# Kernel tuning notes

Measured on AMD Instinct MI355X. Metric: run time of the kernel, lower is better.

## Reference

```python
import jax, jax.numpy as jnp
import numpy as np

# Fixed average-trace buffer from the module (length 120)
AVG = jnp.asarray([0.0256,0.0823,0.1157,0.1315,0.1366,0.1369,0.1347,0.1308,0.1259,0.1205,0.1146,0.1086,0.1028,0.097,0.0913,0.0858,0.0805,0.0756,0.0708,0.0664,0.0623,0.0584,0.0549,0.0515,0.0485,0.0456,0.0429,0.0404,0.0381,0.036,0.034,0.0321,0.0304,0.0287,0.0272,0.0258,0.0245,0.0233,0.0222,0.0211,0.0201,0.0191,0.0182,0.0173,0.0165,0.0158,0.015,0.0143,0.0137,0.013,0.0125,0.0119,0.0114,0.0108,0.0104,0.0099,0.0095,0.0091,0.0087,0.0083,0.008,0.0077,0.0074,0.0071,0.0068,0.0065,0.0062,0.006,0.0058,0.0055,0.0053,0.005,0.0049,0.0047,0.0045,0.0044,0.0042,0.004,0.0039,0.0038,0.0036,0.0034,0.0033,0.0032,0.0031,0.003,0.0029,0.0028,0.0027,0.0026,0.0025,0.0024,0.0023,0.0022,0.0021,0.0021,0.002,0.0019,0.0018,0.0018,0.0017,0.0017,0.0016,0.0016,0.0015,0.0015,0.0014,0.0014,0.0013,0.0013,0.0013,0.0012,0.0012,0.0011,0.0011,0.0011,0.001,0.001,0.001,0.0009], dtype=jnp.float32)


def _lstm(x, w_ih, w_hh, b):
    """PyTorch-semantics single-layer LSTM. x: [N,T,D], w_ih: [4H,D], w_hh: [4H,H], b: [4H] (= b_ih + b_hh). Gate order i,f,g,o."""
    xp = jnp.einsum('ntd,gd->ntg', x, w_ih) + b  # precompute input projections: [N,T,4H]
    N = x.shape[0]
    H = w_hh.shape[1]
    h0 = jnp.zeros((N, H), x.dtype)

    def step(carry, xt):
        h, c = carry
        g = xt + h @ w_hh.T  # [N,4H]
        i, f, gg, o = jnp.split(g, 4, axis=-1)
        c = jax.nn.sigmoid(f) * c + jax.nn.sigmoid(i) * jnp.tanh(gg)
        h = jax.nn.sigmoid(o) * jnp.tanh(c)
        return (h, c), h

    _, hs = jax.lax.scan(step, (h0, h0), jnp.swapaxes(xp, 0, 1))  # hs: [T,N,H]
    return jnp.swapaxes(hs, 0, 1)  # [N,T,H]


def setup_inputs() -> dict:
    key = jax.random.key(0)
    ks = jax.random.split(key, 7)
    N, F, H = 32768, 12, 30
    s1 = 1.0 / float(np.sqrt(H))  # torch LSTM init: U(-1/sqrt(H), 1/sqrt(H))
    s2 = 1.0                      # second LSTM hidden=1 -> scale 1
    return {
        'features': jax.random.normal(ks[0], (N, F), jnp.float32),
        'w_ih1': jax.random.uniform(ks[1], (4 * H, F + 1), jnp.float32, -s1, s1),
        'w_hh1': jax.random.uniform(ks[2], (4 * H, H), jnp.float32, -s1, s1),
        'b1': jax.random.uniform(ks[3], (4 * H,), jnp.float32, -s1, s1),
        'w_ih2': jax.random.uniform(ks[4], (4, H), jnp.float32, -s2, s2),
        'w_hh2': jax.random.uniform(ks[5], (4, 1), jnp.float32, -s2, s2),
        'b2': jax.random.uniform(ks[6], (4,), jnp.float32, -s2, s2),
    }


def reference(features, w_ih1, w_hh1, b1, w_ih2, w_hh2, b2):
    N, F = features.shape
    T = AVG.shape[0]  # 120
    x = jnp.broadcast_to(features[:, None, :], (N, T, F))          # repeat features over time
    trace = jnp.broadcast_to(AVG[None, :, None], (N, T, 1))        # average trace channel
    x = jnp.concatenate([x, trace], axis=2)                        # [N,120,13]
    h1 = _lstm(x, w_ih1, w_hh1, b1)                                # [N,120,30]
    return _lstm(h1, w_ih2, w_hh2, b2)                             # [N,120,1]
```

## Files before the change

### kernel.cpp

```cpp
#include <hip/hip_runtime.h>

typedef __attribute__((ext_vector_type(8))) short bf16x8;
typedef __attribute__((ext_vector_type(4))) float f32x4;

#define LOG2E 1.44269504088896340736f

__device__ __constant__ float AVG_D[120] = {
    0.0256f,0.0823f,0.1157f,0.1315f,0.1366f,0.1369f,0.1347f,0.1308f,0.1259f,0.1205f,
    0.1146f,0.1086f,0.1028f,0.0970f,0.0913f,0.0858f,0.0805f,0.0756f,0.0708f,0.0664f,
    0.0623f,0.0584f,0.0549f,0.0515f,0.0485f,0.0456f,0.0429f,0.0404f,0.0381f,0.0360f,
    0.0340f,0.0321f,0.0304f,0.0287f,0.0272f,0.0258f,0.0245f,0.0233f,0.0222f,0.0211f,
    0.0201f,0.0191f,0.0182f,0.0173f,0.0165f,0.0158f,0.0150f,0.0143f,0.0137f,0.0130f,
    0.0125f,0.0119f,0.0114f,0.0108f,0.0104f,0.0099f,0.0095f,0.0091f,0.0087f,0.0083f,
    0.0080f,0.0077f,0.0074f,0.0071f,0.0068f,0.0065f,0.0062f,0.0060f,0.0058f,0.0055f,
    0.0053f,0.0050f,0.0049f,0.0047f,0.0045f,0.0044f,0.0042f,0.0040f,0.0039f,0.0038f,
    0.0036f,0.0034f,0.0033f,0.0032f,0.0031f,0.0030f,0.0029f,0.0028f,0.0027f,0.0026f,
    0.0025f,0.0024f,0.0023f,0.0022f,0.0021f,0.0021f,0.0020f,0.0019f,0.0018f,0.0018f,
    0.0017f,0.0017f,0.0016f,0.0016f,0.0015f,0.0015f,0.0014f,0.0014f,0.0013f,0.0013f,
    0.0013f,0.0012f,0.0012f,0.0011f,0.0011f,0.0011f,0.0010f,0.0010f,0.0010f,0.0009f
};

__device__ __forceinline__ float sig2(float x) {
    return __builtin_amdgcn_rcpf(1.0f + __builtin_amdgcn_exp2f(x));
}
__device__ __forceinline__ float tanh2(float x) {
    return fmaf(2.0f, __builtin_amdgcn_rcpf(1.0f + __builtin_amdgcn_exp2f(x)), -1.0f);
}
__device__ __forceinline__ unsigned short tb(float x) {
    return (unsigned short)(__float_as_uint(x) >> 16);
}
__device__ __forceinline__ float fb(unsigned short h) {
    return __uint_as_float(((unsigned)h) << 16);
}

__global__ void pack_weights(const float* __restrict__ w_ih1,
                             const float* __restrict__ w_hh1,
                             const float* __restrict__ b1,
                             const float* __restrict__ w_ih2,
                             const float* __restrict__ b2,
                             float* __restrict__ ws) {
    unsigned short* whi = (unsigned short*)ws;
    unsigned short* wlo = (unsigned short*)(ws + 2048);
    float* bconst = ws + 4096;
    float* wih1f  = ws + 4224;
    unsigned* avgpk = (unsigned*)(ws + 5760);
    const int tid = threadIdx.x;
    for (int idx = tid; idx < 4096; idx += 256) {
        const int T = idx >> 9, lane = (idx >> 3) & 63, j = idx & 7;
        const int r = 16 * T + (lane & 15);
        const int k = ((lane >> 4) & 3) * 8 + j;
        const int u = r >> 2, q = r & 3;
        const float sc = (q == 2) ? (-2.0f * LOG2E) : (-LOG2E);
        float v = 0.0f;
        if (u < 30) {
            if (k < 30)       v = w_hh1[(q * 30 + u) * 30 + k];
            else if (k == 30) v = w_ih1[(q * 30 + u) * 13 + 12];
        } else if (u == 30 && k < 30) {
            v = w_ih2[q * 30 + k];
        }
        v *= sc;
        const unsigned short hi = tb(v);
        whi[idx] = hi;
        wlo[idx] = tb(v - fb(hi));
    }
    for (int r = tid; r < 128; r += 256) {
        const int u = r >> 2, q = r & 3;
        const float sc = (q == 2) ? (-2.0f * LOG2E) : (-LOG2E);
        bconst[r] = sc * ((u < 30) ? b1[q * 30 + u] : ((u == 30) ? b2[q] : 0.0f));
    }
    for (int idx = tid; idx < 1536; idx += 256) {
        const int r = idx / 12, d = idx % 12;
        const int u = r >> 2, q = r & 3;
        const float sc = (q == 2) ? (-2.0f * LOG2E) : (-LOG2E);
        wih1f[idx] = (u < 30) ? sc * w_ih1[(q * 30 + u) * 13 + d] : 0.0f;
    }
    for (int t = tid; t < 121; t += 256) {
        const float a = (t < 120) ? AVG_D[t] : 0.0f;
        const unsigned short hi = tb(a);
        const unsigned short lo = tb(a - fb(hi));
        avgpk[t] = (unsigned)hi | ((unsigned)lo << 16);
    }
}

__global__ __launch_bounds__(128, 4)
void lstm_mfma_kernel(const float* __restrict__ feat,
                      const float* __restrict__ w_hh2,
                      const float* __restrict__ ws,
                      float* __restrict__ out) {
    __shared__ __align__(16) unsigned short hhi[2][16 * 40];
    __shared__ __align__(16) unsigned short hlo[2][16 * 40];
    __shared__ __align__(16) float out_s[16 * 124];

    const int tid  = threadIdx.x;
    const int lane = tid & 63;
    const int wv   = __builtin_amdgcn_readfirstlane(tid >> 6) & 1;
    const int s    = lane & 15;
    const int quad = lane >> 4;
    const int seq  = blockIdx.x * 16 + s;
    const unsigned* avgpk = (const unsigned*)(ws + 5760);

    {
        unsigned* zh = (unsigned*)(&hhi[0][0]);
        unsigned* zl = (unsigned*)(&hlo[0][0]);
        for (int i = tid; i < 640; i += 128) { zh[i] = 0u; zl[i] = 0u; }
    }
    __syncthreads();
    if (tid < 16) {
        const unsigned a0 = avgpk[0];
        hhi[0][tid * 40 + 30] = (unsigned short)a0;
        hlo[0][tid * 40 + 30] = (unsigned short)(a0 >> 16);
    }

    bf16x8 Ahi[4], Alo[4];
    {
        const unsigned short* wahi = (const unsigned short*)ws;
        const unsigned short* walo = (const unsigned short*)(ws + 2048);
#pragma unroll
        for (int T = 0; T < 4; T++) {
            const int Tg = 4 * wv + T;
            Ahi[T] = *(const bf16x8*)(wahi + Tg * 512 + lane * 8);
            Alo[T] = *(const bf16x8*)(walo + Tg * 512 + lane * 8);
        }
    }

    float f0[12];
    {
        const float4* fp = reinterpret_cast<const float4*>(feat + seq * 12);
        float4 A = fp[0], B = fp[1], C = fp[2];
        f0[0]=A.x; f0[1]=A.y; f0[2]=A.z; f0[3]=A.w;
        f0[4]=B.x; f0[5]=B.y; f0[6]=B.z; f0[7]=B.w;
        f0[8]=C.x; f0[9]=C.y; f0[10]=C.z; f0[11]=C.w;
    }
    f32x4 projb[4];
    {
        const float* bconst = ws + 4096;
        const float* wih1f  = ws + 4224;
#pragma unroll
        for (int T = 0; T < 4; T++) {
#pragma unroll
            for (int g = 0; g < 4; g++) {
                const int r = 16 * (4 * wv + T) + 4 * quad + g;
                float acc = bconst[r];
#pragma unroll
                for (int d = 0; d < 12; d++) acc = fmaf(f0[d], wih1f[r * 12 + d], acc);
                projb[T][g] = acc;
            }
        }
    }

    float c1[4];
#pragma unroll
    for (int T = 0; T < 4; T++) c1[T] = 0.0f;
    float h2 = 0.0f, c2 = 0.0f;
    const float whs0 = -LOG2E * w_hh2[0];
    const float whs1 = -LOG2E * w_hh2[1];
    const float whs2 = -2.0f * LOG2E * w_hh2[2];
    const float whs3 = -LOG2E * w_hh2[3];

    __syncthreads();

    unsigned apk_cur = avgpk[1];

#pragma unroll 1
    for (int t = 0; t <= 120; t++) {
        const int buf = t & 1;
        const unsigned short* bh = hhi[buf];
        const unsigned short* bl = hlo[buf];
        unsigned short* nh = hhi[buf ^ 1];
        unsigned short* nl = hlo[buf ^ 1];

        const unsigned apk = apk_cur;
        apk_cur = avgpk[(t + 2 <= 120) ? (t + 2) : 120];

        const bf16x8 Bhi = *(const bf16x8*)(bh + s * 40 + 8 * quad);
        const bf16x8 Blo = *(const bf16x8*)(bl + s * 40 + 8 * quad);

        f32x4 D[4];
#pragma unroll
        for (int T = 0; T < 4; T++)
            D[T] = __builtin_amdgcn_mfma_f32_16x16x32_bf16(Alo[T], Bhi, projb[T], 0, 0, 0);
#pragma unroll
        for (int T = 0; T < 4; T++)
            D[T] = __builtin_amdgcn_mfma_f32_16x16x32_bf16(Ahi[T], Blo, D[T], 0, 0, 0);
#pragma unroll
        for (int T = 0; T < 4; T++)
            D[T] = __builtin_amdgcn_mfma_f32_16x16x32_bf16(Ahi[T], Bhi, D[T], 0, 0, 0);

        if (wv == 1 && t >= 1 && quad == 2) {
            const float g0 = fmaf(h2, whs0, D[3][0]);
            const float g1 = fmaf(h2, whs1, D[3][1]);
            const float g2 = fmaf(h2, whs2, D[3][2]);
            const float g3 = fmaf(h2, whs3, D[3][3]);
            c2 = sig2(g1) * c2 + sig2(g0) * tanh2(g2);
            h2 = sig2(g3) * tanh2(c2 * (-2.0f * LOG2E));
            out_s[s * 124 + (t - 1)] = h2;
        }

        if (t < 120) {
            float s2a[4], Ba[4], hka[4];
#pragma unroll
            for (int T = 0; T < 4; T++) {
                const float ei = __builtin_amdgcn_exp2f(D[T][0]);
                const float ef = __builtin_amdgcn_exp2f(D[T][1]);
                const float eg = __builtin_amdgcn_exp2f(D[T][2]);
                const float eo = __builtin_amdgcn_exp2f(D[T][3]);
                const float pi_ = 1.0f + ei, pf = 1.0f + ef;
                const float pg  = 1.0f + eg, po = 1.0f + eo;
                const float pig = pi_ * pg;
                const float num = fmaf(c1[T], pig, (1.0f - eg) * pf);
                const float ck  = num * __builtin_amdgcn_rcpf(pf * pig);
                c1[T] = ck;
                float carg = -2.0f * LOG2E * ck;
                carg = fminf(fmaxf(carg, -20.0f), 20.0f);
                const float ec = __builtin_amdgcn_exp2f(carg);
                s2a[T] = 1.0f - ec;
                Ba[T]  = po * (1.0f + ec);
            }
            {
                const float P01 = __builtin_amdgcn_rcpf(Ba[0] * Ba[1]);
                hka[0] = s2a[0] * (Ba[1] * P01);
                hka[1] = s2a[1] * (Ba[0] * P01);
                const int u3 = 16 * wv + 12 + quad;
                const float B3e = (u3 < 30) ? Ba[3] : 1.0f;
                const float P23 = __builtin_amdgcn_rcpf(Ba[2] * B3e);
                hka[2] = s2a[2] * (B3e * P23);
                hka[3] = s2a[3] * (Ba[2] * P23);
            }
#pragma unroll
            for (int T = 0; T < 4; T++) {
                const int u = 16 * wv + 4 * T + quad;
                const unsigned hbits = __float_as_uint(hka[T]);
                const float rem = hka[T] - __uint_as_float(hbits & 0xffff0000u);
                unsigned hi16 = hbits >> 16;
                unsigned lo16 = __float_as_uint(rem) >> 16;
                if (T == 3) {
                    if (u == 30) { hi16 = apk & 0xffffu; lo16 = apk >> 16; }
                    else if (u == 31) { hi16 = 0u; lo16 = 0u; }
                }
                nh[s * 40 + u] = (unsigned short)hi16;
                nl[s * 40 + u] = (unsigned short)lo16;
            }
            __syncthreads();
        }
    }

    __syncthreads();
    float* outb = out + (size_t)blockIdx.x * 16 * 120;
#pragma unroll
    for (int it = 0; it < 4; it++) {
        const int fi = it * 128 + tid;
        if (fi < 480) {
            const int sq = fi / 30, j = fi % 30;
            const float4 v = *reinterpret_cast<const float4*>(&out_s[sq * 124 + j * 4]);
            *reinterpret_cast<float4*>(&outb[sq * 120 + j * 4]) = v;
        }
    }
}

extern "C" void kernel_launch(void* const* d_in, const int* in_sizes, int n_in,
                              void* d_out, int out_size, void* d_ws, size_t ws_size,
                              hipStream_t stream) {
    (void)in_sizes; (void)n_in; (void)out_size; (void)ws_size;
    const float* feat  = (const float*)d_in[0];
    const float* w_ih1 = (const float*)d_in[1];
    const float* w_hh1 = (const float*)d_in[2];
    const float* b1    = (const float*)d_in[3];
    const float* w_ih2 = (const float*)d_in[4];
    const float* w_hh2 = (const float*)d_in[5];
    const float* b2    = (const float*)d_in[6];
    float* ws  = (float*)d_ws;
    float* out = (float*)d_out;

    hipLaunchKernelGGL(pack_weights, dim3(1), dim3(256), 0, stream,
                       w_ih1, w_hh1, b1, w_ih2, b2, ws);
    hipLaunchKernelGGL(lstm_mfma_kernel, dim3(2048), dim3(128), 0, stream,
                       feat, w_hh2, ws, out);
}
```

Measured before the change: 246.1 us.

## Process two independent 16-sequence groups per block to interleave MFMA chains

Each block now handles 32 sequences as two independent groups A and B. Their MFMA chains and gate math are interleaved inside one timestep, so one barrier per step covers both groups and the serial dependency latency of each group can overlap with the other. Grid size is halved, launch bounds drop to 2 blocks per CU, and the second-layer update moves after the barrier. The cost is roughly double the register and shared-memory use per block, which may lower occupancy.

```diff
diff --git a/kernel.cpp b/kernel.cpp
--- a/kernel.cpp
+++ b/kernel.cpp
@@ -82,33 +82,39 @@
     }
 }
 
-__global__ __launch_bounds__(128, 4)
+__global__ __launch_bounds__(128, 2)
 void lstm_mfma_kernel(const float* __restrict__ feat,
                       const float* __restrict__ w_hh2,
                       const float* __restrict__ ws,
                       float* __restrict__ out) {
-    __shared__ __align__(16) unsigned short hhi[2][16 * 40];
-    __shared__ __align__(16) unsigned short hlo[2][16 * 40];
-    __shared__ __align__(16) float out_s[16 * 124];
+    __shared__ __align__(16) unsigned short hhiA[2][16 * 40];
+    __shared__ __align__(16) unsigned short hloA[2][16 * 40];
+    __shared__ __align__(16) unsigned short hhiB[2][16 * 40];
+    __shared__ __align__(16) unsigned short hloB[2][16 * 40];
+    __shared__ __align__(16) float out_s[32 * 124];
 
     const int tid  = threadIdx.x;
     const int lane = tid & 63;
     const int wv   = __builtin_amdgcn_readfirstlane(tid >> 6) & 1;
     const int s    = lane & 15;
     const int quad = lane >> 4;
-    const int seq  = blockIdx.x * 16 + s;
+    const int seqA = blockIdx.x * 32 + s;
     const unsigned* avgpk = (const unsigned*)(ws + 5760);
 
     {
-        unsigned* zh = (unsigned*)(&hhi[0][0]);
-        unsigned* zl = (unsigned*)(&hlo[0][0]);
-        for (int i = tid; i < 640; i += 128) { zh[i] = 0u; zl[i] = 0u; }
+        unsigned* z0 = (unsigned*)(&hhiA[0][0]);
+        unsigned* z1 = (unsigned*)(&hloA[0][0]);
+        unsigned* z2 = (unsigned*)(&hhiB[0][0]);
+        unsigned* z3 = (unsigned*)(&hloB[0][0]);
+        for (int i = tid; i < 640; i += 128) { z0[i]=0u; z1[i]=0u; z2[i]=0u; z3[i]=0u; }
     }
     __syncthreads();
     if (tid < 16) {
         const unsigned a0 = avgpk[0];
-        hhi[0][tid * 40 + 30] = (unsigned short)a0;
-        hlo[0][tid * 40 + 30] = (unsigned short)(a0 >> 16);
+        hhiA[0][tid * 40 + 30] = (unsigned short)a0;
+        hloA[0][tid * 40 + 30] = (unsigned short)(a0 >> 16);
+        hhiB[0][tid * 40 + 30] = (unsigned short)a0;
+        hloB[0][tid * 40 + 30] = (unsigned short)(a0 >> 16);
     }
 
     bf16x8 Ahi[4], Alo[4];
@@ -123,35 +129,45 @@
         }
     }
 
-    float f0[12];
-    {
-        const float4* fp = reinterpret_cast<const float4*>(feat + seq * 12);
-        float4 A = fp[0], B = fp[1], C = fp[2];
-        f0[0]=A.x; f0[1]=A.y; f0[2]=A.z; f0[3]=A.w;
-        f0[4]=B.x; f0[5]=B.y; f0[6]=B.z; f0[7]=B.w;
-        f0[8]=C.x; f0[9]=C.y; f0[10]=C.z; f0[11]=C.w;
-    }
-    f32x4 projb[4];
+    f32x4 projbA[4], projbB[4];
     {
         const float* bconst = ws + 4096;
         const float* wih1f  = ws + 4224;
+        float f0[12], g0[12];
+        {
+            const float4* fp = reinterpret_cast<const float4*>(feat + seqA * 12);
+            float4 A = fp[0], B = fp[1], C = fp[2];
+            f0[0]=A.x; f0[1]=A.y; f0[2]=A.z; f0[3]=A.w;
+            f0[4]=B.x; f0[5]=B.y; f0[6]=B.z; f0[7]=B.w;
+            f0[8]=C.x; f0[9]=C.y; f0[10]=C.z; f0[11]=C.w;
+            const float4* gp = reinterpret_cast<const float4*>(feat + (seqA + 16) * 12);
+            float4 D_ = gp[0], E = gp[1], F = gp[2];
+            g0[0]=D_.x; g0[1]=D_.y; g0[2]=D_.z; g0[3]=D_.w;
+            g0[4]=E.x; g0[5]=E.y; g0[6]=E.z; g0[7]=E.w;
+            g0[8]=F.x; g0[9]=F.y; g0[10]=F.z; g0[11]=F.w;
+        }
 #pragma unroll
         for (int T = 0; T < 4; T++) {
 #pragma unroll
             for (int g = 0; g < 4; g++) {
                 const int r = 16 * (4 * wv + T) + 4 * quad + g;
-                float acc = bconst[r];
-#pragma unroll
-                for (int d = 0; d < 12; d++) acc = fmaf(f0[d], wih1f[r * 12 + d], acc);
-                projb[T][g] = acc;
-            }
-        }
-    }
-
-    float c1[4];
-#pragma unroll
-    for (int T = 0; T < 4; T++) c1[T] = 0.0f;
-    float h2 = 0.0f, c2 = 0.0f;
+                float accA = bconst[r], accB = bconst[r];
+#pragma unroll
+                for (int d = 0; d < 12; d++) {
+                    const float w = wih1f[r * 12 + d];
+                    accA = fmaf(f0[d], w, accA);
+                    accB = fmaf(g0[d], w, accB);
+                }
+                projbA[T][g] = accA;
+                projbB[T][g] = accB;
+            }
+        }
+    }
+
+    float c1A[4], c1B[4];
+#pragma unroll
+    for (int T = 0; T < 4; T++) { c1A[T] = 0.0f; c1B[T] = 0.0f; }
+    float h2A = 0.0f, c2A = 0.0f, h2B = 0.0f, c2B = 0.0f;
     const float whs0 = -LOG2E * w_hh2[0];
     const float whs1 = -LOG2E * w_hh2[1];
     const float whs2 = -2.0f * LOG2E * w_hh2[2];
@@ -164,59 +180,61 @@
 #pragma unroll 1
     for (int t = 0; t <= 120; t++) {
         const int buf = t & 1;
-        const unsigned short* bh = hhi[buf];
-        const unsigned short* bl = hlo[buf];
-        unsigned short* nh = hhi[buf ^ 1];
-        unsigned short* nl = hlo[buf ^ 1];
+        const unsigned short* bhA = hhiA[buf];
+        const unsigned short* blA = hloA[buf];
+        unsigned short* nhA = hhiA[buf ^ 1];
+        unsigned short* nlA = hloA[buf ^ 1];
+        const unsigned short* bhB = hhiB[buf];
+        const unsigned short* blB = hloB[buf];
+        unsigned short* nhB = hhiB[buf ^ 1];
+        unsigned short* nlB = hloB[buf ^ 1];
 
         const unsigned apk = apk_cur;
         apk_cur = avgpk[(t + 2 <= 120) ? (t + 2) : 120];
 
-        const bf16x8 Bhi = *(const bf16x8*)(bh + s * 40 + 8 * quad);
-        const bf16x8 Blo = *(const bf16x8*)(bl + s * 40 + 8 * quad);
-
-        f32x4 D[4];
-#pragma unroll
-        for (int T = 0; T < 4; T++)
-            D[T] = __builtin_amdgcn_mfma_f32_16x16x32_bf16(Alo[T], Bhi, projb[T], 0, 0, 0);
-#pragma unroll
-        for (int T = 0; T < 4; T++)
-            D[T] = __builtin_amdgcn_mfma_f32_16x16x32_bf16(Ahi[T], Blo, D[T], 0, 0, 0);
-#pragma unroll
-        for (int T = 0; T < 4; T++)
-            D[T] = __builtin_amdgcn_mfma_f32_16x16x32_bf16(Ahi[T], Bhi, D[T], 0, 0, 0);
-
-        if (wv == 1 && t >= 1 && quad == 2) {
-            const float g0 = fmaf(h2, whs0, D[3][0]);
-            const float g1 = fmaf(h2, whs1, D[3][1]);
-            const float g2 = fmaf(h2, whs2, D[3][2]);
-            const float g3 = fmaf(h2, whs3, D[3][3]);
-            c2 = sig2(g1) * c2 + sig2(g0) * tanh2(g2);
-            h2 = sig2(g3) * tanh2(c2 * (-2.0f * LOG2E));
-            out_s[s * 124 + (t - 1)] = h2;
+        const bf16x8 BhiA = *(const bf16x8*)(bhA + s * 40 + 8 * quad);
+        const bf16x8 BloA = *(const bf16x8*)(blA + s * 40 + 8 * quad);
+        const bf16x8 BhiB = *(const bf16x8*)(bhB + s * 40 + 8 * quad);
+        const bf16x8 BloB = *(const bf16x8*)(blB + s * 40 + 8 * quad);
+
+        f32x4 DA[4], DB[4];
+#pragma unroll
+        for (int T = 0; T < 4; T++) {
+            DA[T] = __builtin_amdgcn_mfma_f32_16x16x32_bf16(Alo[T], BhiA, projbA[T], 0, 0, 0);
+            DB[T] = __builtin_amdgcn_mfma_f32_16x16x32_bf16(Alo[T], BhiB, projbB[T], 0, 0, 0);
+        }
+#pragma unroll
+        for (int T = 0; T < 4; T++) {
+            DA[T] = __builtin_amdgcn_mfma_f32_16x16x32_bf16(Ahi[T], BloA, DA[T], 0, 0, 0);
+            DB[T] = __builtin_amdgcn_mfma_f32_16x16x32_bf16(Ahi[T], BloB, DB[T], 0, 0, 0);
+        }
+#pragma unroll
+        for (int T = 0; T < 4; T++) {
+            DA[T] = __builtin_amdgcn_mfma_f32_16x16x32_bf16(Ahi[T], BhiA, DA[T], 0, 0, 0);
+            DB[T] = __builtin_amdgcn_mfma_f32_16x16x32_bf16(Ahi[T], BhiB, DB[T], 0, 0, 0);
         }
 
         if (t < 120) {
-            float s2a[4], Ba[4], hka[4];
-#pragma unroll
-            for (int T = 0; T < 4; T++) {
-                const float ei = __builtin_amdgcn_exp2f(D[T][0]);
-                const float ef = __builtin_amdgcn_exp2f(D[T][1]);
-                const float eg = __builtin_amdgcn_exp2f(D[T][2]);
-                const float eo = __builtin_amdgcn_exp2f(D[T][3]);
-                const float pi_ = 1.0f + ei, pf = 1.0f + ef;
-                const float pg  = 1.0f + eg, po = 1.0f + eo;
-                const float pig = pi_ * pg;
-                const float num = fmaf(c1[T], pig, (1.0f - eg) * pf);
-                const float ck  = num * __builtin_amdgcn_rcpf(pf * pig);
-                c1[T] = ck;
-                float carg = -2.0f * LOG2E * ck;
-                carg = fminf(fmaxf(carg, -20.0f), 20.0f);
-                const float ec = __builtin_amdgcn_exp2f(carg);
-                s2a[T] = 1.0f - ec;
-                Ba[T]  = po * (1.0f + ec);
-            }
             {
+                float s2a[4], Ba[4], hka[4];
+#pragma unroll
+                for (int T = 0; T < 4; T++) {
+                    const float ei = __builtin_amdgcn_exp2f(DA[T][0]);
+                    const float ef = __builtin_amdgcn_exp2f(DA[T][1]);
+                    const float eg = __builtin_amdgcn_exp2f(DA[T][2]);
+                    const float eo = __builtin_amdgcn_exp2f(DA[T][3]);
+                    const float pi_ = 1.0f + ei, pf = 1.0f + ef;
+                    const float pg  = 1.0f + eg, po = 1.0f + eo;
+                    const float pig = pi_ * pg;
+                    const float num = fmaf(c1A[T], pig, (1.0f - eg) * pf);
+                    const float ck  = num * __builtin_amdgcn_rcpf(pf * pig);
+                    c1A[T] = ck;
+                    float carg = -2.0f * LOG2E * ck;
+                    carg = fminf(fmaxf(carg, -20.0f), 20.0f);
+                    const float ec = __builtin_amdgcn_exp2f(carg);
+                    s2a[T] = 1.0f - ec;
+                    Ba[T]  = po * (1.0f + ec);
+                }
                 const float P01 = __builtin_amdgcn_rcpf(Ba[0] * Ba[1]);
                 hka[0] = s2a[0] * (Ba[1] * P01);
                 hka[1] = s2a[1] * (Ba[0] * P01);
@@ -225,31 +243,96 @@
                 const float P23 = __builtin_amdgcn_rcpf(Ba[2] * B3e);
                 hka[2] = s2a[2] * (B3e * P23);
                 hka[3] = s2a[3] * (Ba[2] * P23);
-            }
-#pragma unroll
-            for (int T = 0; T < 4; T++) {
-                const int u = 16 * wv + 4 * T + quad;
-                const unsigned hbits = __float_as_uint(hka[T]);
-                const float rem = hka[T] - __uint_as_float(hbits & 0xffff0000u);
-                unsigned hi16 = hbits >> 16;
-                unsigned lo16 = __float_as_uint(rem) >> 16;
-                if (T == 3) {
-                    if (u == 30) { hi16 = apk & 0xffffu; lo16 = apk >> 16; }
-                    else if (u == 31) { hi16 = 0u; lo16 = 0u; }
-                }
-                nh[s * 40 + u] = (unsigned short)hi16;
-                nl[s * 40 + u] = (unsigned short)lo16;
-            }
-            __syncthreads();
+#pragma unroll
+                for (int T = 0; T < 4; T++) {
+                    const int u = 16 * wv + 4 * T + quad;
+                    const unsigned hbits = __float_as_uint(hka[T]);
+                    const float rem = hka[T] - __uint_as_float(hbits & 0xffff0000u);
+                    unsigned hi16 = hbits >> 16;
+                    unsigned lo16 = __float_as_uint(rem) >> 16;
+                    if (T == 3) {
+                        if (u == 30) { hi16 = apk & 0xffffu; lo16 = apk >> 16; }
+                        else if (u == 31) { hi16 = 0u; lo16 = 0u; }
+                    }
+                    nhA[s * 40 + u] = (unsigned short)hi16;
+                    nlA[s * 40 + u] = (unsigned short)lo16;
+                }
+            }
+            {
+                float s2a[4], Ba[4], hka[4];
+#pragma unroll
+                for (int T = 0; T < 4; T++) {
+                    const float ei = __builtin_amdgcn_exp2f(DB[T][0]);
+                    const float ef = __builtin_amdgcn_exp2f(DB[T][1]);
+                    const float eg = __builtin_amdgcn_exp2f(DB[T][2]);
+                    const float eo = __builtin_amdgcn_exp2f(DB[T][3]);
+                    const float pi_ = 1.0f + ei, pf = 1.0f + ef;
+                    const float pg  = 1.0f + eg, po = 1.0f + eo;
+                    const float pig = pi_ * pg;
+                    const float num = fmaf(c1B[T], pig, (1.0f - eg) * pf);
+                    const float ck  = num * __builtin_amdgcn_rcpf(pf * pig);
+                    c1B[T] = ck;
+                    float carg = -2.0f * LOG2E * ck;
+                    carg = fminf(fmaxf(carg, -20.0f), 20.0f);
+                    const float ec = __builtin_amdgcn_exp2f(carg);
+                    s2a[T] = 1.0f - ec;
+                    Ba[T]  = po * (1.0f + ec);
+                }
+                const float P01 = __builtin_amdgcn_rcpf(Ba[0] * Ba[1]);
+                hka[0] = s2a[0] * (Ba[1] * P01);
+                hka[1] = s2a[1] * (Ba[0] * P01);
+                const int u3 = 16 * wv + 12 + quad;
+                const float B3e = (u3 < 30) ? Ba[3] : 1.0f;
+                const float P23 = __builtin_amdgcn_rcpf(Ba[2] * B3e);
+                hka[2] = s2a[2] * (B3e * P23);
+                hka[3] = s2a[3] * (Ba[2] * P23);
+#pragma unroll
+                for (int T = 0; T < 4; T++) {
+                    const int u = 16 * wv + 4 * T + quad;
+                    const unsigned hbits = __float_as_uint(hka[T]);
+                    const float rem = hka[T] - __uint_as_float(hbits & 0xffff0000u);
+                    unsigned hi16 = hbits >> 16;
+                    unsigned lo16 = __float_as_uint(rem) >> 16;
+                    if (T == 3) {
+                        if (u == 30) { hi16 = apk & 0xffffu; lo16 = apk >> 16; }
+                        else if (u == 31) { hi16 = 0u; lo16 = 0u; }
+                    }
+                    nhB[s * 40 + u] = (unsigned short)hi16;
+                    nlB[s * 40 + u] = (unsigned short)lo16;
+                }
+            }
+        }
+
+        __syncthreads();
+
+        if (wv == 1 && t >= 1 && quad == 2) {
+            {
+                const float g0 = fmaf(h2A, whs0, DA[3][0]);
+                const float g1 = fmaf(h2A, whs1, DA[3][1]);
+                const float g2 = fmaf(h2A, whs2, DA[3][2]);
+                const float g3 = fmaf(h2A, whs3, DA[3][3]);
+                c2A = sig2(g1) * c2A + sig2(g0) * tanh2(g2);
+                h2A = sig2(g3) * tanh2(c2A * (-2.0f * LOG2E));
+                out_s[s * 124 + (t - 1)] = h2A;
+            }
+            {
+                const float g0 = fmaf(h2B, whs0, DB[3][0]);
+                const float g1 = fmaf(h2B, whs1, DB[3][1]);
+                const float g2 = fmaf(h2B, whs2, DB[3][2]);
+                const float g3 = fmaf(h2B, whs3, DB[3][3]);
+                c2B = sig2(g1) * c2B + sig2(g0) * tanh2(g2);
+                h2B = sig2(g3) * tanh2(c2B * (-2.0f * LOG2E));
+                out_s[(16 + s) * 124 + (t - 1)] = h2B;
+            }
         }
     }
 
     __syncthreads();
-    float* outb = out + (size_t)blockIdx.x * 16 * 120;
-#pragma unroll
-    for (int it = 0; it < 4; it++) {
+    float* outb = out + (size_t)blockIdx.x * 32 * 120;
+#pragma unroll
+    for (int it = 0; it < 8; it++) {
         const int fi = it * 128 + tid;
-        if (fi < 480) {
+        if (fi < 960) {
             const int sq = fi / 30, j = fi % 30;
             const float4 v = *reinterpret_cast<const float4*>(&out_s[sq * 124 + j * 4]);
             *reinterpret_cast<float4*>(&outb[sq * 120 + j * 4]) = v;
@@ -273,6 +356,6 @@
 
     hipLaunchKernelGGL(pack_weights, dim3(1), dim3(256), 0, stream,
                        w_ih1, w_hh1, b1, w_ih2, b2, ws);
-    hipLaunchKernelGGL(lstm_mfma_kernel, dim3(2048), dim3(128), 0, stream,
+    hipLaunchKernelGGL(lstm_mfma_kernel, dim3(1024), dim3(128), 0, stream,
                        feat, w_hh2, ws, out);
 }
```

Measured after the change: 267.9 us. +8.9%, slower.

## Rebalance gate tiles 5/3 across waves and interleave MFMA with gate math

Applied to the files above, without the earlier changes.

Before, each of the two waves handled four 16-row gate tiles. Now wave 0 takes five tiles and wave 1 takes three, since wave 1 also runs the second LSTM cell. Each tile's three MFMAs are followed right away by its gate activation and hidden-state store, so transcendental work can overlap with later MFMA issue. The layer-2 step now runs after the barrier, and a fmed3 clamp replaces the min/max pair. The imbalanced split and the serialized dependency chain per tile could lengthen the critical path of wave 0.

```diff
diff --git a/kernel.cpp b/kernel.cpp
--- a/kernel.cpp
+++ b/kernel.cpp
@@ -111,15 +111,18 @@
         hlo[0][tid * 40 + 30] = (unsigned short)(a0 >> 16);
     }
 
-    bf16x8 Ahi[4], Alo[4];
+    const int NT = (wv == 0) ? 5 : 3;
+    const int TB = (wv == 0) ? 0 : 5;
+    bf16x8 Ahi[5], Alo[5];
     {
         const unsigned short* wahi = (const unsigned short*)ws;
         const unsigned short* walo = (const unsigned short*)(ws + 2048);
 #pragma unroll
-        for (int T = 0; T < 4; T++) {
-            const int Tg = 4 * wv + T;
-            Ahi[T] = *(const bf16x8*)(wahi + Tg * 512 + lane * 8);
-            Alo[T] = *(const bf16x8*)(walo + Tg * 512 + lane * 8);
+        for (int T = 0; T < 5; T++) {
+            if (T < NT) {
+                Ahi[T] = *(const bf16x8*)(wahi + (TB + T) * 512 + lane * 8);
+                Alo[T] = *(const bf16x8*)(walo + (TB + T) * 512 + lane * 8);
+            }
         }
     }
 
@@ -131,26 +134,28 @@
         f0[4]=B.x; f0[5]=B.y; f0[6]=B.z; f0[7]=B.w;
         f0[8]=C.x; f0[9]=C.y; f0[10]=C.z; f0[11]=C.w;
     }
-    f32x4 projb[4];
+    f32x4 projb[5];
     {
         const float* bconst = ws + 4096;
         const float* wih1f  = ws + 4224;
 #pragma unroll
-        for (int T = 0; T < 4; T++) {
-#pragma unroll
-            for (int g = 0; g < 4; g++) {
-                const int r = 16 * (4 * wv + T) + 4 * quad + g;
-                float acc = bconst[r];
-#pragma unroll
-                for (int d = 0; d < 12; d++) acc = fmaf(f0[d], wih1f[r * 12 + d], acc);
-                projb[T][g] = acc;
-            }
-        }
-    }
-
-    float c1[4];
-#pragma unroll
-    for (int T = 0; T < 4; T++) c1[T] = 0.0f;
+        for (int T = 0; T < 5; T++) {
+            if (T < NT) {
+#pragma unroll
+                for (int g = 0; g < 4; g++) {
+                    const int r = 16 * (TB + T) + 4 * quad + g;
+                    float acc = bconst[r];
+#pragma unroll
+                    for (int d = 0; d < 12; d++) acc = fmaf(f0[d], wih1f[r * 12 + d], acc);
+                    projb[T][g] = acc;
+                }
+            }
+        }
+    }
+
+    float c1[5];
+#pragma unroll
+    for (int T = 0; T < 5; T++) c1[T] = 0.0f;
     float h2 = 0.0f, c2 = 0.0f;
     const float whs0 = -LOG2E * w_hh2[0];
     const float whs1 = -LOG2E * w_hh2[1];
@@ -160,6 +165,35 @@
     __syncthreads();
 
     unsigned apk_cur = avgpk[1];
+
+#define TRIO(Tl) ({ \
+        f32x4 d_ = __builtin_amdgcn_mfma_f32_16x16x32_bf16(Alo[Tl], Bhi, projb[Tl], 0, 0, 0); \
+        d_ = __builtin_amdgcn_mfma_f32_16x16x32_bf16(Ahi[Tl], Blo, d_, 0, 0, 0); \
+        __builtin_amdgcn_mfma_f32_16x16x32_bf16(Ahi[Tl], Bhi, d_, 0, 0, 0); })
+
+#define GATES(dv, Tl) do { \
+        const float ei_ = __builtin_amdgcn_exp2f(dv[0]); \
+        const float ef_ = __builtin_amdgcn_exp2f(dv[1]); \
+        const float eg_ = __builtin_amdgcn_exp2f(dv[2]); \
+        const float eo_ = __builtin_amdgcn_exp2f(dv[3]); \
+        const float pf_ = 1.0f + ef_; \
+        const float pig_ = (1.0f + ei_) * (1.0f + eg_); \
+        const float num_ = fmaf(c1[Tl], pig_, (1.0f - eg_) * pf_); \
+        const float ck_ = num_ * __builtin_amdgcn_rcpf(pf_ * pig_); \
+        c1[Tl] = ck_; \
+        const float carg_ = __builtin_amdgcn_fmed3f(-2.0f * LOG2E * ck_, -20.0f, 20.0f); \
+        const float ec_ = __builtin_amdgcn_exp2f(carg_); \
+        s2a[Tl] = 1.0f - ec_; \
+        Ba[Tl]  = (1.0f + eo_) * (1.0f + ec_); \
+    } while (0)
+
+#define STOREH(hkv, u_) do { \
+        const float hk_ = (hkv); \
+        const unsigned hb_ = __float_as_uint(hk_); \
+        const float rem_ = hk_ - __uint_as_float(hb_ & 0xffff0000u); \
+        nh[s * 40 + (u_)] = (unsigned short)(hb_ >> 16); \
+        nl[s * 40 + (u_)] = (unsigned short)(__float_as_uint(rem_) >> 16); \
+    } while (0)
 
 #pragma unroll 1
     for (int t = 0; t <= 120; t++) {
@@ -175,72 +209,68 @@
         const bf16x8 Bhi = *(const bf16x8*)(bh + s * 40 + 8 * quad);
         const bf16x8 Blo = *(const bf16x8*)(bl + s * 40 + 8 * quad);
 
-        f32x4 D[4];
-#pragma unroll
-        for (int T = 0; T < 4; T++)
-            D[T] = __builtin_amdgcn_mfma_f32_16x16x32_bf16(Alo[T], Bhi, projb[T], 0, 0, 0);
-#pragma unroll
-        for (int T = 0; T < 4; T++)
-            D[T] = __builtin_amdgcn_mfma_f32_16x16x32_bf16(Ahi[T], Blo, D[T], 0, 0, 0);
-#pragma unroll
-        for (int T = 0; T < 4; T++)
-            D[T] = __builtin_amdgcn_mfma_f32_16x16x32_bf16(Ahi[T], Bhi, D[T], 0, 0, 0);
+        float s2a[5], Ba[5];
+        f32x4 Dlast;
+
+        if (wv == 0) {
+            f32x4 d0 = TRIO(0);
+            if (t < 120) GATES(d0, 0);
+            f32x4 d1 = TRIO(1);
+            if (t < 120) {
+                GATES(d1, 1);
+                const float P = __builtin_amdgcn_rcpf(Ba[0] * Ba[1]);
+                STOREH(s2a[0] * (Ba[1] * P), 0 + quad);
+                STOREH(s2a[1] * (Ba[0] * P), 4 + quad);
+            }
+            f32x4 d2 = TRIO(2);
+            if (t < 120) GATES(d2, 2);
+            f32x4 d3 = TRIO(3);
+            if (t < 120) {
+                GATES(d3, 3);
+                const float P = __builtin_amdgcn_rcpf(Ba[2] * Ba[3]);
+                STOREH(s2a[2] * (Ba[3] * P), 8 + quad);
+                STOREH(s2a[3] * (Ba[2] * P), 12 + quad);
+            }
+            f32x4 d4 = TRIO(4);
+            if (t < 120) {
+                GATES(d4, 4);
+                STOREH(s2a[4] * __builtin_amdgcn_rcpf(Ba[4]), 16 + quad);
+            }
+        } else {
+            f32x4 d0 = TRIO(0);
+            if (t < 120) GATES(d0, 0);
+            f32x4 d1 = TRIO(1);
+            if (t < 120) {
+                GATES(d1, 1);
+                const float P = __builtin_amdgcn_rcpf(Ba[0] * Ba[1]);
+                STOREH(s2a[0] * (Ba[1] * P), 20 + quad);
+                STOREH(s2a[1] * (Ba[0] * P), 24 + quad);
+            }
+            Dlast = TRIO(2);
+            if (t < 120) {
+                GATES(Dlast, 2);
+                const float hk = s2a[2] * __builtin_amdgcn_rcpf(Ba[2]);
+                const unsigned hb = __float_as_uint(hk);
+                const float rem = hk - __uint_as_float(hb & 0xffff0000u);
+                unsigned hi16 = hb >> 16;
+                unsigned lo16 = __float_as_uint(rem) >> 16;
+                if (quad == 2) { hi16 = apk & 0xffffu; lo16 = apk >> 16; }
+                else if (quad == 3) { hi16 = 0u; lo16 = 0u; }
+                nh[s * 40 + 28 + quad] = (unsigned short)hi16;
+                nl[s * 40 + 28 + quad] = (unsigned short)lo16;
+            }
+        }
+
+        if (t < 120) __syncthreads();
 
         if (wv == 1 && t >= 1 && quad == 2) {
-            const float g0 = fmaf(h2, whs0, D[3][0]);
-            const float g1 = fmaf(h2, whs1, D[3][1]);
-            const float g2 = fmaf(h2, whs2, D[3][2]);
-            const float g3 = fmaf(h2, whs3, D[3][3]);
+            const float g0 = fmaf(h2, whs0, Dlast[0]);
+            const float g1 = fmaf(h2, whs1, Dlast[1]);
+            const float g2 = fmaf(h2, whs2, Dlast[2]);
+            const float g3 = fmaf(h2, whs3, Dlast[3]);
             c2 = sig2(g1) * c2 + sig2(g0) * tanh2(g2);
             h2 = sig2(g3) * tanh2(c2 * (-2.0f * LOG2E));
             out_s[s * 124 + (t - 1)] = h2;
-        }
-
-        if (t < 120) {
-            float s2a[4], Ba[4], hka[4];
-#pragma unroll
-            for (int T = 0; T < 4; T++) {
-                const float ei = __builtin_amdgcn_exp2f(D[T][0]);
-                const float ef = __builtin_amdgcn_exp2f(D[T][1]);
-                const float eg = __builtin_amdgcn_exp2f(D[T][2]);
-                const float eo = __builtin_amdgcn_exp2f(D[T][3]);
-                const float pi_ = 1.0f + ei, pf = 1.0f + ef;
-                const float pg  = 1.0f + eg, po = 1.0f + eo;
-                const float pig = pi_ * pg;
-                const float num = fmaf(c1[T], pig, (1.0f - eg) * pf);
-                const float ck  = num * __builtin_amdgcn_rcpf(pf * pig);
-                c1[T] = ck;
-                float carg = -2.0f * LOG2E * ck;
-                carg = fminf(fmaxf(carg, -20.0f), 20.0f);
-                const float ec = __builtin_amdgcn_exp2f(carg);
-                s2a[T] = 1.0f - ec;
-                Ba[T]  = po * (1.0f + ec);
-            }
-            {
-                const float P01 = __builtin_amdgcn_rcpf(Ba[0] * Ba[1]);
-                hka[0] = s2a[0] * (Ba[1] * P01);
-                hka[1] = s2a[1] * (Ba[0] * P01);
-                const int u3 = 16 * wv + 12 + quad;
-                const float B3e = (u3 < 30) ? Ba[3] : 1.0f;
-                const float P23 = __builtin_amdgcn_rcpf(Ba[2] * B3e);
-                hka[2] = s2a[2] * (B3e * P23);
-                hka[3] = s2a[3] * (Ba[2] * P23);
-            }
-#pragma unroll
-            for (int T = 0; T < 4; T++) {
-                const int u = 16 * wv + 4 * T + quad;
-                const unsigned hbits = __float_as_uint(hka[T]);
-                const float rem = hka[T] - __uint_as_float(hbits & 0xffff0000u);
-                unsigned hi16 = hbits >> 16;
-                unsigned lo16 = __float_as_uint(rem) >> 16;
-                if (T == 3) {
-                    if (u == 30) { hi16 = apk & 0xffffu; lo16 = apk >> 16; }
-                    else if (u == 31) { hi16 = 0u; lo16 = 0u; }
-                }
-                nh[s * 40 + u] = (unsigned short)hi16;
-                nl[s * 40 + u] = (unsigned short)lo16;
-            }
-            __syncthreads();
         }
     }
 
```

Measured after the change: 267.4 us. 1.09x slower.
